# Optimization experiments

Hardware: AMD Instinct MI355X
Metric: run time of the kernel (lower is better)

## Reference

```python
import jax, jax.numpy as jnp
import numpy as np

N_NODES = 100000


def _gcn_conv(x, W, b, src, dst, norm):
    # x: [N, Fin] -> [N, Fout]; PyG GCNConv: linear, normalized scatter-add, bias
    x = x @ W
    msgs = x[src] * norm[:, None]  # gather + edge scale
    out = jax.ops.segment_sum(msgs, dst, num_segments=N_NODES)
    return out + b


def setup_inputs() -> dict:
    key = jax.random.key(0)
    ks = jax.random.split(key, 8)
    N, E, F, H, C = N_NODES, 600000, 128, 128, 40
    s = lambda fan: 1.0 / np.sqrt(fan)
    return {
        "features": jax.random.normal(ks[0], (N, F), dtype=jnp.float32),
        "edge_index": jax.random.randint(ks[1], (2, E), 0, N, dtype=jnp.int64),
        "W1": jax.random.normal(ks[2], (F, H), dtype=jnp.float32) * s(F),
        "b1": jnp.zeros((H,), dtype=jnp.float32),
        "W2": jax.random.normal(ks[3], (H, H), dtype=jnp.float32) * s(H),
        "b2": jnp.zeros((H,), dtype=jnp.float32),
        "W3": jax.random.normal(ks[4], (H, C), dtype=jnp.float32) * s(H),
        "b3": jnp.zeros((C,), dtype=jnp.float32),
    }


def reference(features, edge_index, W1, b1, W2, b2, W3, b3):
    N = N_NODES
    # add self-loops (PyG GCNConv default)
    loops = jnp.arange(N, dtype=edge_index.dtype)
    src = jnp.concatenate([edge_index[0], loops])
    dst = jnp.concatenate([edge_index[1], loops])
    # symmetric normalization: deg^-1/2[src] * deg^-1/2[dst]
    deg = jax.ops.segment_sum(jnp.ones_like(dst, dtype=features.dtype), dst,
                              num_segments=N)
    dis = jnp.where(deg > 0, jax.lax.rsqrt(jnp.maximum(deg, 1.0)), 0.0)
    norm = dis[src] * dis[dst]

    x = jax.nn.relu(_gcn_conv(features, W1, b1, src, dst, norm))
    x = jax.nn.relu(_gcn_conv(x, W2, b2, src, dst, norm))
    x = jax.nn.relu(_gcn_conv(x, W3, b3, src, dst, norm))
    return jax.nn.log_softmax(x, axis=-1)
```

## Files before the change

kernel.cpp:

```cpp
#include <hip/hip_runtime.h>
#include <hip/hip_bf16.h>

#define NN 100000
#define NE 600000
#define NBLK 391
#define NPAD 100096

typedef unsigned int uint;
typedef unsigned short ushort;
typedef __attribute__((ext_vector_type(8))) short bf16x8;
typedef __attribute__((ext_vector_type(4))) float f32x4;

__device__ __forceinline__ ushort f2b(float f) {
    union { float f; uint u; } v; v.f = f;
    return (ushort)((v.u + 0x7fffu + ((v.u >> 16) & 1u)) >> 16);
}
__device__ __forceinline__ uint f2b2(float lo, float hi) {
    return (uint)f2b(lo) | ((uint)f2b(hi) << 16);
}
__device__ __forceinline__ float b2f(uint h) {
    union { uint u; float f; } v; v.u = h << 16; return v.f;
}

__global__ __launch_bounds__(256) void k_init_castW(int* __restrict__ cnt,
                                                    const float* __restrict__ W1,
                                                    const float* __restrict__ W2,
                                                    const float* __restrict__ W3,
                                                    ushort* __restrict__ WTall) {
    int t = threadIdx.x;
    if (blockIdx.x < NBLK) {
        int i = blockIdx.x * 256 + t;
        if (i < NN) cnt[i] = 0;
    } else {
        int o = (blockIdx.x - NBLK) * 256 + t;
        if (o >= 38912) return;
        float v;
        if (o < 32768) {
            const float* W = (o < 16384) ? W1 : W2;
            int off = o & 16383;
            int n = off >> 7, k = off & 127;
            v = W[k * 128 + n];
        } else {
            int off = o - 32768;
            int n = off >> 7, k = off & 127;
            v = (n < 40) ? W3[k * 40 + n] : 0.f;
        }
        WTall[o] = f2b(v);
    }
}
__global__ __launch_bounds__(256) void k_cnt(const int* __restrict__ dst,
                                             int* __restrict__ cnt,
                                             int* __restrict__ rank) {
    int e = blockIdx.x * 256 + threadIdx.x;
    if (e < NE) rank[e] = atomicAdd(&cnt[dst[e]], 1);
}
__global__ __launch_bounds__(256) void k_blockred(const int* __restrict__ cnt,
                                                  int* __restrict__ blocksum) {
    int t = threadIdx.x;
    int i = blockIdx.x * 256 + t;
    int c = (i < NN) ? cnt[i] : 0;
    #pragma unroll
    for (int o = 32; o; o >>= 1) c += __shfl_xor(c, o, 64);
    __shared__ int ws[4];
    if ((t & 63) == 0) ws[t >> 6] = c;
    __syncthreads();
    if (t == 0) blocksum[blockIdx.x] = ws[0] + ws[1] + ws[2] + ws[3];
}
__global__ __launch_bounds__(256) void k_scanblk(const int* __restrict__ blocksum,
                                                 int* __restrict__ blockbase) {
    __shared__ int s[NBLK];
    int t = threadIdx.x;
    for (int i = t; i < NBLK; i += 256) s[i] = blocksum[i];
    __syncthreads();
    if (t == 0) {
        int run = 0;
        for (int i = 0; i < NBLK; ++i) { int v = s[i]; s[i] = run; run += v; }
    }
    __syncthreads();
    for (int i = t; i < NBLK; i += 256) blockbase[i] = s[i];
}
__global__ __launch_bounds__(256) void k_offsets(const int* __restrict__ cnt,
                                                 const int* __restrict__ blockbase,
                                                 int* __restrict__ offsets,
                                                 float* __restrict__ dis) {
    int t = threadIdx.x, lane = t & 63, wv = t >> 6;
    int i = blockIdx.x * 256 + t;
    int c = (i < NN) ? cnt[i] : 0;
    int x = c;
    #pragma unroll
    for (int o = 1; o < 64; o <<= 1) {
        int v = __shfl_up(x, o, 64);
        if (lane >= o) x += v;
    }
    __shared__ int wsum[4], wbase[4];
    if (lane == 63) wsum[wv] = x;
    __syncthreads();
    if (t == 0) {
        int run = 0;
        #pragma unroll
        for (int k = 0; k < 4; ++k) { wbase[k] = run; run += wsum[k]; }
    }
    __syncthreads();
    int excl = blockbase[blockIdx.x] + wbase[wv] + x - c;
    if (i < NN) {
        offsets[i] = excl;
        dis[i] = rsqrtf((float)(c + 1));
        if (i == NN - 1) offsets[NN] = excl + c;
    }
}
__global__ __launch_bounds__(256) void k_fill(const int* __restrict__ src,
                                              const int* __restrict__ dst,
                                              const int* __restrict__ rank,
                                              const int* __restrict__ offsets,
                                              int* __restrict__ edges) {
    int e = blockIdx.x * 256 + threadIdx.x;
    if (e < NE) {
        int s = src[e], d = dst[e], r = rank[e];
        edges[offsets[d] + r] = s;
    }
}

__global__ __launch_bounds__(256, 4) void k_gemm1(const float* __restrict__ Xf,
                                                  const ushort* __restrict__ WT,
                                                  const float* __restrict__ dis,
                                                  ushort* __restrict__ Yb) {
    __shared__ ushort AL[64 * 136];
    __shared__ ushort BL[64 * 136];
    const int t = threadIdx.x;
    const int rbase = blockIdx.x * 64;
    if (blockIdx.x == 0 && t < 16) {
        uint4 z = make_uint4(0, 0, 0, 0);
        ((uint4*)(Yb + (size_t)NN * 128))[t] = z;
    }
    #pragma unroll
    for (int i = 0; i < 4; ++i) {
        int ch = t + 256 * i;
        int n = ch >> 4, c = ch & 15;
        *(int4*)(BL + n * 136 + c * 8) = *(const int4*)(WT + n * 128 + c * 8);
    }
    #pragma unroll
    for (int i = 0; i < 4; ++i) {
        int ch = t + 256 * i;
        int m = ch >> 4, c = ch & 15;
        int row = min(rbase + m, NN - 1);
        float4 f0 = *(const float4*)(Xf + (size_t)row * 128 + c * 8);
        float4 f1 = *(const float4*)(Xf + (size_t)row * 128 + c * 8 + 4);
        uint4 o;
        o.x = f2b2(f0.x, f0.y);
        o.y = f2b2(f0.z, f0.w);
        o.z = f2b2(f1.x, f1.y);
        o.w = f2b2(f1.z, f1.w);
        *(uint4*)(AL + m * 136 + c * 8) = o;
    }
    __syncthreads();
    const int wv = t >> 6, l = t & 63;
    const int m16 = l & 15, q = l >> 4;
    f32x4 acc[8];
    #pragma unroll
    for (int j = 0; j < 8; ++j) acc[j] = (f32x4){0.f, 0.f, 0.f, 0.f};
    #pragma unroll
    for (int kt = 0; kt < 4; ++kt) {
        bf16x8 a = *(const bf16x8*)(AL + (wv * 16 + m16) * 136 + kt * 32 + q * 8);
        #pragma unroll
        for (int j = 0; j < 4; ++j) {
            bf16x8 b = *(const bf16x8*)(BL + (j * 16 + m16) * 136 + kt * 32 + q * 8);
            acc[j] = __builtin_amdgcn_mfma_f32_16x16x32_bf16(a, b, acc[j], 0, 0, 0);
        }
    }
    __syncthreads();
    #pragma unroll
    for (int i = 0; i < 4; ++i) {
        int ch = t + 256 * i;
        int n = ch >> 4, c = ch & 15;
        *(int4*)(BL + n * 136 + c * 8) = *(const int4*)(WT + (64 + n) * 128 + c * 8);
    }
    __syncthreads();
    #pragma unroll
    for (int kt = 0; kt < 4; ++kt) {
        bf16x8 a = *(const bf16x8*)(AL + (wv * 16 + m16) * 136 + kt * 32 + q * 8);
        #pragma unroll
        for (int j = 0; j < 4; ++j) {
            bf16x8 b = *(const bf16x8*)(BL + (j * 16 + m16) * 136 + kt * 32 + q * 8);
            acc[4 + j] = __builtin_amdgcn_mfma_f32_16x16x32_bf16(a, b, acc[4 + j], 0, 0, 0);
        }
    }
    #pragma unroll
    for (int r = 0; r < 4; ++r) {
        int row = rbase + wv * 16 + q * 4 + r;
        if (row < NN) {
            float ds = dis[row];
            #pragma unroll
            for (int j = 0; j < 8; ++j)
                Yb[(size_t)row * 128 + j * 16 + m16] = f2b(acc[j][r] * ds);
        }
    }
}

__global__ __launch_bounds__(256, 4) void k_fused128(const int* __restrict__ offsets,
                                                     const int* __restrict__ edges,
                                                     const float* __restrict__ dis,
                                                     const ushort* __restrict__ xw,
                                                     const float* __restrict__ bias,
                                                     const ushort* __restrict__ WT,
                                                     ushort* __restrict__ out) {
    __shared__ ushort AL[64 * 136];
    __shared__ ushort BL[64 * 136];
    const int t = threadIdx.x;
    const int rbase = blockIdx.x * 64;
    if (blockIdx.x == 0 && t < 16) {
        uint4 z = make_uint4(0, 0, 0, 0);
        ((uint4*)(out + (size_t)NN * 128))[t] = z;
    }
    #pragma unroll
    for (int i = 0; i < 4; ++i) {
        int ch = t + 256 * i;
        int n = ch >> 4, c = ch & 15;
        *(int4*)(BL + n * 136 + c * 8) = *(const int4*)(WT + n * 128 + c * 8);
    }
    const int wv = t >> 6, lane = t & 63;
    const int hl = lane & 15;
    const int qsel = lane & 48;
    const int qid = wv * 4 + (lane >> 4);
    #pragma unroll
    for (int iter = 0; iter < 4; ++iter) {
        const int m = qid * 4 + iter;
        const int n = rbase + m;
        const int nc = min(n, NN - 1);
        const int beg = offsets[nc], end = offsets[nc + 1];
        const int deg = end - beg;
        int s_l = (hl < deg) ? edges[beg + hl] : NN;
        uint4 v0 = ((const uint4*)(xw + (size_t)nc * 128))[hl];
        float a0 = b2f(v0.x & 0xffffu), a1 = b2f(v0.x >> 16);
        float a2 = b2f(v0.y & 0xffffu), a3 = b2f(v0.y >> 16);
        float a4 = b2f(v0.z & 0xffffu), a5 = b2f(v0.z >> 16);
        float a6 = b2f(v0.w & 0xffffu), a7 = b2f(v0.w >> 16);
        int degc = min(deg, 16);
        int qceil = (degc + 7) & ~7;
        int m1 = max(degc, __shfl_xor(degc, 16, 64));
        int dmax = max(m1, __shfl_xor(m1, 32, 64));
        int jceil = (dmax + 7) & ~7;
        for (int j = 0; j < jceil; j += 8) {
            if (j < qceil) {
                int s[8]; uint4 u[8];
                #pragma unroll
                for (int k = 0; k < 8; ++k) s[k] = __shfl(s_l, qsel + j + k, 64);
                #pragma unroll
                for (int k = 0; k < 8; ++k)
                    u[k] = ((const uint4*)(xw + (size_t)s[k] * 128))[hl];
                #pragma unroll
                for (int k = 0; k < 8; ++k) {
                    a0 += b2f(u[k].x & 0xffffu); a1 += b2f(u[k].x >> 16);
                    a2 += b2f(u[k].y & 0xffffu); a3 += b2f(u[k].y >> 16);
                    a4 += b2f(u[k].z & 0xffffu); a5 += b2f(u[k].z >> 16);
                    a6 += b2f(u[k].w & 0xffffu); a7 += b2f(u[k].w >> 16);
                }
            }
        }
        for (int jj = beg + 16; jj < end; ++jj) {
            int s2 = edges[jj];
            uint4 u = ((const uint4*)(xw + (size_t)s2 * 128))[hl];
            a0 += b2f(u.x & 0xffffu); a1 += b2f(u.x >> 16);
            a2 += b2f(u.y & 0xffffu); a3 += b2f(u.y >> 16);
            a4 += b2f(u.z & 0xffffu); a5 += b2f(u.z >> 16);
            a6 += b2f(u.w & 0xffffu); a7 += b2f(u.w >> 16);
        }
        float d = dis[nc];
        float4 bv0 = ((const float4*)bias)[2 * hl];
        float4 bv1 = ((const float4*)bias)[2 * hl + 1];
        a0 = fmaxf(fmaf(a0, d, bv0.x), 0.f); a1 = fmaxf(fmaf(a1, d, bv0.y), 0.f);
        a2 = fmaxf(fmaf(a2, d, bv0.z), 0.f); a3 = fmaxf(fmaf(a3, d, bv0.w), 0.f);
        a4 = fmaxf(fmaf(a4, d, bv1.x), 0.f); a5 = fmaxf(fmaf(a5, d, bv1.y), 0.f);
        a6 = fmaxf(fmaf(a6, d, bv1.z), 0.f); a7 = fmaxf(fmaf(a7, d, bv1.w), 0.f);
        uint4 o;
        o.x = f2b2(a0, a1);
        o.y = f2b2(a2, a3);
        o.z = f2b2(a4, a5);
        o.w = f2b2(a6, a7);
        *(uint4*)(AL + m * 136 + hl * 8) = o;
    }
    __syncthreads();
    const int m16 = lane & 15, q = lane >> 4;
    f32x4 acc[8];
    #pragma unroll
    for (int j = 0; j < 8; ++j) acc[j] = (f32x4){0.f, 0.f, 0.f, 0.f};
    #pragma unroll
    for (int kt = 0; kt < 4; ++kt) {
        bf16x8 a = *(const bf16x8*)(AL + (wv * 16 + m16) * 136 + kt * 32 + q * 8);
        #pragma unroll
        for (int j = 0; j < 4; ++j) {
            bf16x8 b = *(const bf16x8*)(BL + (j * 16 + m16) * 136 + kt * 32 + q * 8);
            acc[j] = __builtin_amdgcn_mfma_f32_16x16x32_bf16(a, b, acc[j], 0, 0, 0);
        }
    }
    __syncthreads();
    #pragma unroll
    for (int i = 0; i < 4; ++i) {
        int ch = t + 256 * i;
        int n = ch >> 4, c = ch & 15;
        *(int4*)(BL + n * 136 + c * 8) = *(const int4*)(WT + (64 + n) * 128 + c * 8);
    }
    __syncthreads();
    #pragma unroll
    for (int kt = 0; kt < 4; ++kt) {
        bf16x8 a = *(const bf16x8*)(AL + (wv * 16 + m16) * 136 + kt * 32 + q * 8);
        #pragma unroll
        for (int j = 0; j < 4; ++j) {
            bf16x8 b = *(const bf16x8*)(BL + (j * 16 + m16) * 136 + kt * 32 + q * 8);
            acc[4 + j] = __builtin_amdgcn_mfma_f32_16x16x32_bf16(a, b, acc[4 + j], 0, 0, 0);
        }
    }
    #pragma unroll
    for (int r = 0; r < 4; ++r) {
        int row = rbase + wv * 16 + q * 4 + r;
        if (row < NN) {
            float ds = dis[row];
            #pragma unroll
            for (int j = 0; j < 8; ++j)
                out[(size_t)row * 128 + j * 16 + m16] = f2b(acc[j][r] * ds);
        }
    }
}

__global__ __launch_bounds__(256, 5) void k_fused40(const int* __restrict__ offsets,
                                                    const int* __restrict__ edges,
                                                    const float* __restrict__ dis,
                                                    const ushort* __restrict__ xw,
                                                    const float* __restrict__ bias,
                                                    const ushort* __restrict__ W3T,
                                                    ushort* __restrict__ out) {
    __shared__ ushort AL[64 * 136];
    __shared__ ushort BL[48 * 136];
    const int t = threadIdx.x;
    const int rbase = blockIdx.x * 64;
    if (blockIdx.x == 0 && t < 8) {
        uint4 z = make_uint4(0, 0, 0, 0);
        ((uint4*)(out + (size_t)NN * 64))[t] = z;
    }
    #pragma unroll
    for (int i = 0; i < 3; ++i) {
        int ch = t + 256 * i;
        int n = ch >> 4, c = ch & 15;
        *(int4*)(BL + n * 136 + c * 8) = *(const int4*)(W3T + n * 128 + c * 8);
    }
    const int wv = t >> 6, lane = t & 63;
    const int hl = lane & 15;
    const int qsel = lane & 48;
    const int qid = wv * 4 + (lane >> 4);
    #pragma unroll
    for (int iter = 0; iter < 4; ++iter) {
        const int m = qid * 4 + iter;
        const int n = rbase + m;
        const int nc = min(n, NN - 1);
        const int beg = offsets[nc], end = offsets[nc + 1];
        const int deg = end - beg;
        int s_l = (hl < deg) ? edges[beg + hl] : NN;
        uint4 v0 = ((const uint4*)(xw + (size_t)nc * 128))[hl];
        float a0 = b2f(v0.x & 0xffffu), a1 = b2f(v0.x >> 16);
        float a2 = b2f(v0.y & 0xffffu), a3 = b2f(v0.y >> 16);
        float a4 = b2f(v0.z & 0xffffu), a5 = b2f(v0.z >> 16);
        float a6 = b2f(v0.w & 0xffffu), a7 = b2f(v0.w >> 16);
        int degc = min(deg, 16);
        int qceil = (degc + 7) & ~7;
        int m1 = max(degc, __shfl_xor(degc, 16, 64));
        int dmax = max(m1, __shfl_xor(m1, 32, 64));
        int jceil = (dmax + 7) & ~7;
        for (int j = 0; j < jceil; j += 8) {
            if (j < qceil) {
                int s[8]; uint4 u[8];
                #pragma unroll
                for (int k = 0; k < 8; ++k) s[k] = __shfl(s_l, qsel + j + k, 64);
                #pragma unroll
                for (int k = 0; k < 8; ++k)
                    u[k] = ((const uint4*)(xw + (size_t)s[k] * 128))[hl];
                #pragma unroll
                for (int k = 0; k < 8; ++k) {
                    a0 += b2f(u[k].x & 0xffffu); a1 += b2f(u[k].x >> 16);
                    a2 += b2f(u[k].y & 0xffffu); a3 += b2f(u[k].y >> 16);
                    a4 += b2f(u[k].z & 0xffffu); a5 += b2f(u[k].z >> 16);
                    a6 += b2f(u[k].w & 0xffffu); a7 += b2f(u[k].w >> 16);
                }
            }
        }
        for (int jj = beg + 16; jj < end; ++jj) {
            int s2 = edges[jj];
            uint4 u = ((const uint4*)(xw + (size_t)s2 * 128))[hl];
            a0 += b2f(u.x & 0xffffu); a1 += b2f(u.x >> 16);
            a2 += b2f(u.y & 0xffffu); a3 += b2f(u.y >> 16);
            a4 += b2f(u.z & 0xffffu); a5 += b2f(u.z >> 16);
            a6 += b2f(u.w & 0xffffu); a7 += b2f(u.w >> 16);
        }
        float d = dis[nc];
        float4 bv0 = ((const float4*)bias)[2 * hl];
        float4 bv1 = ((const float4*)bias)[2 * hl + 1];
        a0 = fmaxf(fmaf(a0, d, bv0.x), 0.f); a1 = fmaxf(fmaf(a1, d, bv0.y), 0.f);
        a2 = fmaxf(fmaf(a2, d, bv0.z), 0.f); a3 = fmaxf(fmaf(a3, d, bv0.w), 0.f);
        a4 = fmaxf(fmaf(a4, d, bv1.x), 0.f); a5 = fmaxf(fmaf(a5, d, bv1.y), 0.f);
        a6 = fmaxf(fmaf(a6, d, bv1.z), 0.f); a7 = fmaxf(fmaf(a7, d, bv1.w), 0.f);
        uint4 o;
        o.x = f2b2(a0, a1);
        o.y = f2b2(a2, a3);
        o.z = f2b2(a4, a5);
        o.w = f2b2(a6, a7);
        *(uint4*)(AL + m * 136 + hl * 8) = o;
    }
    __syncthreads();
    const int m16 = lane & 15, q = lane >> 4;
    f32x4 acc[3];
    #pragma unroll
    for (int j = 0; j < 3; ++j) acc[j] = (f32x4){0.f, 0.f, 0.f, 0.f};
    #pragma unroll
    for (int kt = 0; kt < 4; ++kt) {
        bf16x8 a = *(const bf16x8*)(AL + (wv * 16 + m16) * 136 + kt * 32 + q * 8);
        #pragma unroll
        for (int j = 0; j < 3; ++j) {
            bf16x8 b = *(const bf16x8*)(BL + (j * 16 + m16) * 136 + kt * 32 + q * 8);
            acc[j] = __builtin_amdgcn_mfma_f32_16x16x32_bf16(a, b, acc[j], 0, 0, 0);
        }
    }
    #pragma unroll
    for (int r = 0; r < 4; ++r) {
        int row = rbase + wv * 16 + q * 4 + r;
        if (row < NN) {
            float ds = dis[row];
            #pragma unroll
            for (int j = 0; j < 3; ++j)
                out[(size_t)row * 64 + j * 16 + m16] = f2b(acc[j][r] * ds);
        }
    }
}

__global__ __launch_bounds__(256) void k_agg40_lsm(const int* __restrict__ offsets,
                                                   const int* __restrict__ edges,
                                                   const float* __restrict__ dis,
                                                   const ushort* __restrict__ xw,
                                                   const float* __restrict__ bias,
                                                   float* __restrict__ out) {
    const int t = threadIdx.x;
    const int wv = t >> 6, lane = t & 63;
    const int hl = lane & 15;
    const int qsel = lane & 48;
    const int n = (blockIdx.x * 4 + wv) * 4 + (lane >> 4);
    const bool nvalid = n < NN;
    const int nc = nvalid ? n : NN - 1;
    const bool act = hl < 10;
    const int beg = offsets[nc], end = offsets[nc + 1];
    const int deg = end - beg;
    int s_l = (hl < deg) ? edges[beg + hl] : NN;
    uint2 v0 = ((const uint2*)(xw + (size_t)nc * 64))[hl];
    float x0 = b2f(v0.x & 0xffffu), x1 = b2f(v0.x >> 16);
    float x2 = b2f(v0.y & 0xffffu), x3 = b2f(v0.y >> 16);
    int degc = min(deg, 16);
    int qceil = (degc + 7) & ~7;
    int m1 = max(degc, __shfl_xor(degc, 16, 64));
    int dmax = max(m1, __shfl_xor(m1, 32, 64));
    int jceil = (dmax + 7) & ~7;
    for (int j = 0; j < jceil; j += 8) {
        if (j < qceil) {
            int s[8]; uint2 u[8];
            #pragma unroll
            for (int k = 0; k < 8; ++k) s[k] = __shfl(s_l, qsel + j + k, 64);
            #pragma unroll
            for (int k = 0; k < 8; ++k)
                u[k] = ((const uint2*)(xw + (size_t)s[k] * 64))[hl];
            #pragma unroll
            for (int k = 0; k < 8; ++k) {
                x0 += b2f(u[k].x & 0xffffu); x1 += b2f(u[k].x >> 16);
                x2 += b2f(u[k].y & 0xffffu); x3 += b2f(u[k].y >> 16);
            }
        }
    }
    for (int jj = beg + 16; jj < end; ++jj) {
        int s2 = edges[jj];
        uint2 u = ((const uint2*)(xw + (size_t)s2 * 64))[hl];
        x0 += b2f(u.x & 0xffffu); x1 += b2f(u.x >> 16);
        x2 += b2f(u.y & 0xffffu); x3 += b2f(u.y >> 16);
    }
    float d = dis[nc];
    if (act) {
        float4 bv = ((const float4*)bias)[hl];
        x0 = fmaxf(fmaf(x0, d, bv.x), 0.f);
        x1 = fmaxf(fmaf(x1, d, bv.y), 0.f);
        x2 = fmaxf(fmaf(x2, d, bv.z), 0.f);
        x3 = fmaxf(fmaf(x3, d, bv.w), 0.f);
    }
    float m = act ? fmaxf(fmaxf(x0, x1), fmaxf(x2, x3)) : -1e30f;
    #pragma unroll
    for (int o = 8; o; o >>= 1) m = fmaxf(m, __shfl_xor(m, o, 64));
    float e = act ? (expf(x0 - m) + expf(x1 - m) + expf(x2 - m) + expf(x3 - m)) : 0.f;
    #pragma unroll
    for (int o = 8; o; o >>= 1) e += __shfl_xor(e, o, 64);
    if (act && nvalid) {
        float lg = m + logf(e);
        float4 o4 = make_float4(x0 - lg, x1 - lg, x2 - lg, x3 - lg);
        *(float4*)(out + (size_t)n * 40 + 4 * hl) = o4;
    }
}

extern "C" void kernel_launch(void* const* d_in, const int* in_sizes, int n_in,
                              void* d_out, int out_size, void* d_ws, size_t ws_size,
                              hipStream_t stream) {
    const float* feat = (const float*)d_in[0];
    const int* ei = (const int*)d_in[1];
    const float* W1 = (const float*)d_in[2];
    const float* b1 = (const float*)d_in[3];
    const float* W2 = (const float*)d_in[4];
    const float* b2 = (const float*)d_in[5];
    const float* W3 = (const float*)d_in[6];
    const float* b3 = (const float*)d_in[7];
    const int* src = ei;
    const int* dst = ei + NE;
    float* out = (float*)d_out;

    char* w = (char*)d_ws;
    int* cnt = (int*)w;        w += 100352 * 4;
    float* dis = (float*)w;    w += 100352 * 4;
    int* offsets = (int*)w;    w += 100608 * 4;
    int* rank = (int*)w;       w += 600064 * 4;
    int* blocksum = (int*)w;   w += 512 * 4;
    int* blockbase = (int*)w;  w += 512 * 4;
    int* edges = (int*)w;      w += 600064 * 4;
    ushort* WTall = (ushort*)w; w += 39168 * 2;
    ushort* W1T = WTall;
    ushort* W2T = WTall + 16384;
    ushort* W3T = WTall + 32768;
    ushort* bufYb = (ushort*)w; w += (size_t)NPAD * 128 * 2;
    ushort* bufXb = (ushort*)w; w += (size_t)NPAD * 128 * 2;
    ushort* Y40b = (ushort*)w;  w += (size_t)NPAD * 64 * 2;

    const int B = 256;
    #define CDIV(a, b) (((a) + (b) - 1) / (b))

    k_init_castW<<<NBLK + CDIV(38912, B), B, 0, stream>>>(cnt, W1, W2, W3, WTall);
    k_cnt<<<CDIV(NE, B), B, 0, stream>>>(dst, cnt, rank);
    k_blockred<<<NBLK, B, 0, stream>>>(cnt, blocksum);
    k_scanblk<<<1, B, 0, stream>>>(blocksum, blockbase);
    k_offsets<<<NBLK, B, 0, stream>>>(cnt, blockbase, offsets, dis);
    k_fill<<<CDIV(NE, B), B, 0, stream>>>(src, dst, rank, offsets, edges);

    k_gemm1<<<CDIV(NN, 64), B, 0, stream>>>(feat, W1T, dis, bufYb);
    k_fused128<<<CDIV(NN, 64), B, 0, stream>>>(offsets, edges, dis, bufYb, b1, W2T, bufXb);
    k_fused40<<<CDIV(NN, 64), B, 0, stream>>>(offsets, edges, dis, bufXb, b2, W3T, Y40b);
    k_agg40_lsm<<<CDIV(NN, 16), B, 0, stream>>>(offsets, edges, dis, Y40b, b3, out);
    #undef CDIV
}
```

Before: 240.2 us.

## Fold block scan into offsets kernel and shrink fused128 weight tile

Removes the single-block serial scan kernel by having each offsets block sum its preceding block totals directly with a strided reduction. This drops one launch and its serial latency at the cost of redundant reads of the small blocksum array. In k_fused128 the weight LDS tile is halved and streamed in four 32-row passes with the launch bound raised to 6 blocks per CU. The smaller LDS footprint is meant to allow more resident blocks, in exchange for extra barriers and weight reloads.

```diff
diff --git a/kernel.cpp b/kernel.cpp
--- a/kernel.cpp
+++ b/kernel.cpp
@@ -66,25 +66,22 @@
     __syncthreads();
     if (t == 0) blocksum[blockIdx.x] = ws[0] + ws[1] + ws[2] + ws[3];
 }
-__global__ __launch_bounds__(256) void k_scanblk(const int* __restrict__ blocksum,
-                                                 int* __restrict__ blockbase) {
-    __shared__ int s[NBLK];
-    int t = threadIdx.x;
-    for (int i = t; i < NBLK; i += 256) s[i] = blocksum[i];
-    __syncthreads();
-    if (t == 0) {
-        int run = 0;
-        for (int i = 0; i < NBLK; ++i) { int v = s[i]; s[i] = run; run += v; }
-    }
-    __syncthreads();
-    for (int i = t; i < NBLK; i += 256) blockbase[i] = s[i];
-}
 __global__ __launch_bounds__(256) void k_offsets(const int* __restrict__ cnt,
-                                                 const int* __restrict__ blockbase,
+                                                 const int* __restrict__ blocksum,
                                                  int* __restrict__ offsets,
                                                  float* __restrict__ dis) {
     int t = threadIdx.x, lane = t & 63, wv = t >> 6;
-    int i = blockIdx.x * 256 + t;
+    const int bid = blockIdx.x;
+    __shared__ int red[4];
+    int part = 0;
+    for (int i = t; i < bid; i += 256) part += blocksum[i];
+    #pragma unroll
+    for (int o = 32; o; o >>= 1) part += __shfl_xor(part, o, 64);
+    if (lane == 0) red[wv] = part;
+    __syncthreads();
+    int base = red[0] + red[1] + red[2] + red[3];
+
+    int i = bid * 256 + t;
     int c = (i < NN) ? cnt[i] : 0;
     int x = c;
     #pragma unroll
@@ -101,7 +98,7 @@
         for (int k = 0; k < 4; ++k) { wbase[k] = run; run += wsum[k]; }
     }
     __syncthreads();
-    int excl = blockbase[blockIdx.x] + wbase[wv] + x - c;
+    int excl = base + wbase[wv] + x - c;
     if (i < NN) {
         offsets[i] = excl;
         dis[i] = rsqrtf((float)(c + 1));
@@ -196,7 +193,7 @@
     }
 }
 
-__global__ __launch_bounds__(256, 4) void k_fused128(const int* __restrict__ offsets,
+__global__ __launch_bounds__(256, 6) void k_fused128(const int* __restrict__ offsets,
                                                      const int* __restrict__ edges,
                                                      const float* __restrict__ dis,
                                                      const ushort* __restrict__ xw,
@@ -204,7 +201,7 @@
                                                      const ushort* __restrict__ WT,
                                                      ushort* __restrict__ out) {
     __shared__ ushort AL[64 * 136];
-    __shared__ ushort BL[64 * 136];
+    __shared__ ushort BL[32 * 136];
     const int t = threadIdx.x;
     const int rbase = blockIdx.x * 64;
     if (blockIdx.x == 0 && t < 16) {
@@ -212,7 +209,7 @@
         ((uint4*)(out + (size_t)NN * 128))[t] = z;
     }
     #pragma unroll
-    for (int i = 0; i < 4; ++i) {
+    for (int i = 0; i < 2; ++i) {
         int ch = t + 256 * i;
         int n = ch >> 4, c = ch & 15;
         *(int4*)(BL + n * 136 + c * 8) = *(const int4*)(WT + n * 128 + c * 8);
@@ -284,29 +281,27 @@
     #pragma unroll
     for (int j = 0; j < 8; ++j) acc[j] = (f32x4){0.f, 0.f, 0.f, 0.f};
     #pragma unroll
-    for (int kt = 0; kt < 4; ++kt) {
-        bf16x8 a = *(const bf16x8*)(AL + (wv * 16 + m16) * 136 + kt * 32 + q * 8);
+    for (int p = 0; p < 4; ++p) {
+        if (p > 0) {
+            __syncthreads();
+            #pragma unroll
+            for (int i = 0; i < 2; ++i) {
+                int ch = t + 256 * i;
+                int n = ch >> 4, c = ch & 15;
+                *(int4*)(BL + n * 136 + c * 8) =
+                    *(const int4*)(WT + (p * 32 + n) * 128 + c * 8);
+            }
+            __syncthreads();
+        }
         #pragma unroll
-        for (int j = 0; j < 4; ++j) {
-            bf16x8 b = *(const bf16x8*)(BL + (j * 16 + m16) * 136 + kt * 32 + q * 8);
-            acc[j] = __builtin_amdgcn_mfma_f32_16x16x32_bf16(a, b, acc[j], 0, 0, 0);
-        }
-    }
-    __syncthreads();
-    #pragma unroll
-    for (int i = 0; i < 4; ++i) {
-        int ch = t + 256 * i;
-        int n = ch >> 4, c = ch & 15;
-        *(int4*)(BL + n * 136 + c * 8) = *(const int4*)(WT + (64 + n) * 128 + c * 8);
-    }
-    __syncthreads();
-    #pragma unroll
-    for (int kt = 0; kt < 4; ++kt) {
-        bf16x8 a = *(const bf16x8*)(AL + (wv * 16 + m16) * 136 + kt * 32 + q * 8);
-        #pragma unroll
-        for (int j = 0; j < 4; ++j) {
-            bf16x8 b = *(const bf16x8*)(BL + (j * 16 + m16) * 136 + kt * 32 + q * 8);
-            acc[4 + j] = __builtin_amdgcn_mfma_f32_16x16x32_bf16(a, b, acc[4 + j], 0, 0, 0);
+        for (int kt = 0; kt < 4; ++kt) {
+            bf16x8 a = *(const bf16x8*)(AL + (wv * 16 + m16) * 136 + kt * 32 + q * 8);
+            #pragma unroll
+            for (int jj = 0; jj < 2; ++jj) {
+                bf16x8 b = *(const bf16x8*)(BL + (jj * 16 + m16) * 136 + kt * 32 + q * 8);
+                acc[p * 2 + jj] =
+                    __builtin_amdgcn_mfma_f32_16x16x32_bf16(a, b, acc[p * 2 + jj], 0, 0, 0);
+            }
         }
     }
     #pragma unroll
@@ -517,7 +512,6 @@
     int* offsets = (int*)w;    w += 100608 * 4;
     int* rank = (int*)w;       w += 600064 * 4;
     int* blocksum = (int*)w;   w += 512 * 4;
-    int* blockbase = (int*)w;  w += 512 * 4;
     int* edges = (int*)w;      w += 600064 * 4;
     ushort* WTall = (ushort*)w; w += 39168 * 2;
     ushort* W1T = WTall;
@@ -533,8 +527,7 @@
     k_init_castW<<<NBLK + CDIV(38912, B), B, 0, stream>>>(cnt, W1, W2, W3, WTall);
     k_cnt<<<CDIV(NE, B), B, 0, stream>>>(dst, cnt, rank);
     k_blockred<<<NBLK, B, 0, stream>>>(cnt, blocksum);
-    k_scanblk<<<1, B, 0, stream>>>(blocksum, blockbase);
-    k_offsets<<<NBLK, B, 0, stream>>>(cnt, blockbase, offsets, dis);
+    k_offsets<<<NBLK, B, 0, stream>>>(cnt, blocksum, offsets, dis);
     k_fill<<<CDIV(NE, B), B, 0, stream>>>(src, dst, rank, offsets, edges);
 
     k_gemm1<<<CDIV(NN, 64), B, 0, stream>>>(feat, W1T, dis, bufYb);
```

New measurement: 249.0 us. +3.6%, slower.
